# Performance work log

Measured on AMD Instinct MI355X. Metric: run time of the kernel, lower is better.

## Reference

```python
import jax, jax.numpy as jnp
import numpy as np

NO = 16          # config['Max_Object']
NT = 8           # config['Max_Time']
FEAT = 512       # config['feat_dims']
VIS_IN = 2048
TGT = 24


def setup_inputs() -> dict:
    key = jax.random.key(0)
    ks = jax.random.split(key, 10)
    b = 16
    N = NT * 2 * NO  # 256
    s = lambda k, *sh: jax.random.normal(k, sh, dtype=jnp.float32) * 0.02
    return {
        "src": jax.random.normal(ks[0], (b, 1, 1, N, VIS_IN), dtype=jnp.float32),
        "tgt_rel": jax.random.randint(ks[1], (b * NT * NO * NO,), 0, TGT, dtype=jnp.int64),
        "w1": s(ks[2], VIS_IN, FEAT), "b1": jnp.zeros((FEAT,), jnp.float32),
        "w2": s(ks[3], FEAT, FEAT),   "b2": jnp.zeros((FEAT,), jnp.float32),
        "wf": s(ks[4], FEAT, FEAT),   "bf": jnp.zeros((FEAT,), jnp.float32),
        "wr": s(ks[5], 2 * FEAT, TGT), "br": jnp.zeros((TGT,), jnp.float32),
    }


def reference(src, tgt_rel, w1, b1, w2, b2, wf, bf, wr, br):
    b = src.shape[0]
    BT = b * NT
    # src[:, 0, 0, :, :] -> (b, N, D) -> (b*NT, 2*NO, D); take visual part [:2048]
    x = src[:, 0, 0, :, :].reshape(BT, 2 * NO, -1)[:, :, :VIS_IN]
    # fc_vis: MLP 2048 -> FEAT -> FEAT
    h = jnp.maximum(x @ w1 + b1, 0.0) @ w2 + b2          # (BT, 2NO, FEAT)
    node_feats = h @ wf + bf                             # fc_fusion
    # vectorized replacement of the NOxNO python double loop:
    # edge[:, i*NO + (j-NO), :] = cat(node[:, i], node[:, j])  for i<NO<=j
    subj = jnp.broadcast_to(node_feats[:, :NO, None, :], (BT, NO, NO, FEAT))
    obj = jnp.broadcast_to(node_feats[:, None, NO:, :], (BT, NO, NO, FEAT))
    edge_feats = jnp.concatenate([subj, obj], axis=-1).reshape(BT, NO * NO, 2 * FEAT)
    out = (edge_feats @ wr + br).reshape(-1, TGT)        # fc_rel
    tgt = tgt_rel.reshape(-1)
    w_cls = jnp.asarray([1.0] + [100.0] * (TGT - 1), dtype=out.dtype)
    logp = jax.nn.log_softmax(out, axis=-1)
    nll = -jnp.take_along_axis(logp, tgt[:, None], axis=1)[:, 0]
    ww = w_cls[tgt]
    loss = jnp.sum(ww * nll) / jnp.sum(ww)  # torch weighted cross_entropy (mean)
    return out, tgt, loss
```

## Files before the change

### kernel.cpp

```cpp
#include <hip/hip_runtime.h>
#include <cstddef>
#include <cstdint>

#define NOBJ   16
#define FEAT   512
#define VIS    2048
#define NTGT   24
#define MROWS  4096
#define EROWS  32768

typedef __attribute__((ext_vector_type(8))) short short8;
typedef __attribute__((ext_vector_type(4))) float f32x4;

__device__ __forceinline__ unsigned short f2bf(float f) {
    union { float f; unsigned int i; } v; v.f = f;
    const unsigned int x = v.i;
    return (unsigned short)((x + 0x7fffu + ((x >> 16) & 1u)) >> 16);
}

__device__ __forceinline__ void gload16(const unsigned short* g, unsigned short* l) {
    __builtin_amdgcn_global_load_lds(
        (const __attribute__((address_space(1))) unsigned int*)(const void*)g,
        (__attribute__((address_space(3))) unsigned int*)(void*)l, 16, 0, 0);
}

__global__ __launch_bounds__(256)
void prep1(const float* __restrict__ w1, unsigned short* __restrict__ w1t,
           const float* __restrict__ wf, const float* __restrict__ bfv,
           const float* __restrict__ wr, float* __restrict__ t1,
           const float* __restrict__ src, unsigned short* __restrict__ srcb) {
    __shared__ float shbuf[FEAT * NTGT];
    const int b   = blockIdx.x;
    const int tid = threadIdx.x;
    if (b < 1024) {
        float (*tile)[33] = (float(*)[33])shbuf;
        const int k0 = (b & 63) * 32;
        const int n0 = (b >> 6) * 32;
        const int tx = tid & 31, ty = tid >> 5;
        #pragma unroll
        for (int r = 0; r < 32; r += 8)
            tile[ty + r][tx] = w1[(size_t)(k0 + ty + r) * FEAT + n0 + tx];
        __syncthreads();
        #pragma unroll
        for (int r = 0; r < 32; r += 8)
            w1t[(size_t)(n0 + ty + r) * VIS + k0 + tx] = f2bf(tile[tx][ty + r]);
    } else if (b < 1154) {
        const int bb = b - 1024;
        const int h  = bb & 1;
        const float* wrh = wr + (size_t)h * FEAT * NTGT;
        for (int idx = tid; idx < FEAT * NTGT; idx += 256)
            shbuf[idx] = wrh[idx];
        __syncthreads();
        const int c    = tid & 31;
        const int krow = (bb >> 1) * 8 + (tid >> 5);
        if (krow > 512) return;
        const float* rowp = (krow < 512) ? (wf + (size_t)krow * FEAT) : bfv;
        const int ce = (c < NTGT) ? c : NTGT - 1;
        float s = 0.f;
        #pragma unroll 8
        for (int j = 0; j < FEAT; ++j)
            s = fmaf(rowp[j], shbuf[j * NTGT + ce], s);
        if (c < NTGT) t1[((size_t)h * 513 + krow) * 32 + c] = s;
    } else {
        const int bb = b - 1154;
        #pragma unroll
        for (int q = 0; q < 4; ++q) {
            const size_t i = (size_t)bb * 8192 + q * 2048 + tid * 8;
            const float4 a = *reinterpret_cast<const float4*>(src + i);
            const float4 c = *reinterpret_cast<const float4*>(src + i + 4);
            short8 o;
            o[0] = (short)f2bf(a.x); o[1] = (short)f2bf(a.y);
            o[2] = (short)f2bf(a.z); o[3] = (short)f2bf(a.w);
            o[4] = (short)f2bf(c.x); o[5] = (short)f2bf(c.y);
            o[6] = (short)f2bf(c.z); o[7] = (short)f2bf(c.w);
            *reinterpret_cast<short8*>(srcb + i) = o;
        }
    }
}

__global__ __launch_bounds__(256)
void prep2(const float* __restrict__ w2, const float* __restrict__ b2,
           const float* __restrict__ t1, unsigned short* __restrict__ wABt,
           float* __restrict__ biasAB, float* __restrict__ P) {
    __shared__ float shbuf[FEAT * NTGT];
    const int b   = blockIdx.x;
    const int tid = threadIdx.x;
    if (b < 1024) {
        P[(size_t)b * 256 + tid] = 0.f;
        return;
    }
    const int bb = b - 1024;
    const int h  = bb & 1;
    for (int idx = tid; idx < FEAT * NTGT; idx += 256) {
        const int row = idx / NTGT, col = idx - row * NTGT;
        shbuf[idx] = t1[((size_t)h * 513 + row) * 32 + col];
    }
    __syncthreads();
    const int c = tid & 31;
    const int r = (bb >> 1) * 8 + (tid >> 5);
    if (r > 512) return;
    const float* rowp = (r < 512) ? (w2 + (size_t)r * FEAT) : b2;
    const int ce = (c < NTGT) ? c : NTGT - 1;
    float s = 0.f;
    #pragma unroll 8
    for (int k = 0; k < FEAT; ++k)
        s = fmaf(rowp[k], shbuf[k * NTGT + ce], s);
    if (c < NTGT) {
        const int q = h * NTGT + c;
        if (r < 512) wABt[(size_t)q * FEAT + r] = f2bf(s);
        else         biasAB[q] = s + t1[((size_t)h * 513 + 512) * 32 + c];
    }
}

__global__ __launch_bounds__(256)
void gemm1f(const unsigned short* __restrict__ srcb, const unsigned short* __restrict__ w1t,
            const float* __restrict__ b1, const unsigned short* __restrict__ wABt,
            float* __restrict__ P) {
    __shared__ __align__(16) unsigned short As[2][64 * 64];
    __shared__ __align__(16) unsigned short Bs[2][32 * 64];

    const int bid = blockIdx.x;
    const int xcd = bid & 7;
    const int k8  = bid >> 3;
    const int xb  = k8 & 15;
    const int yb  = (xcd << 3) | (k8 >> 4);
    const int m0 = yb * 64;
    const int n0 = xb * 32;

    const int tid  = threadIdx.x;
    const int lane = tid & 63;
    const int wid  = tid >> 6;
    const int wr = wid >> 1, wc = wid & 1;

    const int aRow0 = tid >> 3, aCd0 = (tid & 7) ^ (aRow0 & 7);
    const int s1i   = 256 + tid;
    const int aRow1 = s1i >> 3, aCd1 = (s1i & 7) ^ (aRow1 & 7);
    const int bN    = tid >> 3, bCd = (tid & 7) ^ (bN & 7);
    const size_t aOff0 = (size_t)(m0 + aRow0) * VIS + (aCd0 << 3);
    const size_t aOff1 = (size_t)(m0 + aRow1) * VIS + (aCd1 << 3);
    const size_t bOff  = (size_t)(n0 + bN) * VIS + (bCd << 3);
    const int ldsA0 = (wid * 64) << 3;
    const int ldsA1 = (256 + wid * 64) << 3;
    const int ldsB  = (wid * 64) << 3;

    f32x4 acc[2] = {};

    gload16(srcb + aOff0, &As[0][ldsA0]);
    gload16(srcb + aOff1, &As[0][ldsA1]);
    gload16(w1t + bOff,  &Bs[0][ldsB]);
    __syncthreads();

    int cur = 0;
    for (int t = 0; t < VIS / 64; ++t) {
        if (t + 1 < VIS / 64) {
            const int kn = (t + 1) * 64;
            gload16(srcb + aOff0 + kn, &As[cur ^ 1][ldsA0]);
            gload16(srcb + aOff1 + kn, &As[cur ^ 1][ldsA1]);
            gload16(w1t + bOff + kn,  &Bs[cur ^ 1][ldsB]);
        }
        #pragma unroll
        for (int k2 = 0; k2 < 2; ++k2) {
            short8 af[2], bfr;
            #pragma unroll
            for (int fr = 0; fr < 2; ++fr) {
                const int row = wr * 32 + fr * 16 + (lane & 15);
                const int cw  = ((k2 << 2) + (lane >> 4)) ^ (row & 7);
                af[fr] = *reinterpret_cast<const short8*>(&As[cur][(row << 6) + (cw << 3)]);
            }
            {
                const int n  = wc * 16 + (lane & 15);
                const int cw = ((k2 << 2) + (lane >> 4)) ^ (n & 7);
                bfr = *reinterpret_cast<const short8*>(&Bs[cur][(n << 6) + (cw << 3)]);
            }
            #pragma unroll
            for (int fr = 0; fr < 2; ++fr)
                acc[fr] = __builtin_amdgcn_mfma_f32_16x16x32_bf16(af[fr], bfr, acc[fr], 0, 0, 0);
        }
        __syncthreads();
        cur ^= 1;
    }

    short8 bq[3];
    #pragma unroll
    for (int t3 = 0; t3 < 3; ++t3)
        bq[t3] = *reinterpret_cast<const short8*>(
            wABt + (size_t)(t3 * 16 + (lane & 15)) * FEAT + n0 + ((lane >> 4) << 3));

    unsigned short* Ht = &As[0][0];
    {
        const int nl   = wc * 16 + (lane & 15);
        const float bias = b1[n0 + nl];
        #pragma unroll
        for (int fr = 0; fr < 2; ++fr) {
            const int ml = wr * 32 + fr * 16 + ((lane >> 4) << 2);
            #pragma unroll
            for (int r = 0; r < 4; ++r) {
                const float v = fmaxf(acc[fr][r] + bias, 0.f);
                Ht[(ml + r) * 40 + nl] = f2bf(v);
            }
        }
    }
    __syncthreads();

    short8 aep;
    {
        const int m = wid * 16 + (lane & 15);
        aep = *reinterpret_cast<const short8*>(&Ht[m * 40 + ((lane >> 4) << 3)]);
    }
    const f32x4 pz = {0.f, 0.f, 0.f, 0.f};
    #pragma unroll
    for (int t3 = 0; t3 < 3; ++t3) {
        f32x4 pp = __builtin_amdgcn_mfma_f32_16x16x32_bf16(aep, bq[t3], pz, 0, 0, 0);
        const int q  = t3 * 16 + (lane & 15);
        const int mb = m0 + wid * 16 + ((lane >> 4) << 2);
        #pragma unroll
        for (int r = 0; r < 4; ++r)
            atomicAdd(&P[(size_t)(mb + r) * 64 + q], pp[r]);
    }
}

__global__ __launch_bounds__(256)
void out_loss_kernel(const float* __restrict__ P, const float* __restrict__ br,
                     const float* __restrict__ biasAB, const int* __restrict__ tgt,
                     float* __restrict__ out, float* __restrict__ out_tgt,
                     float* __restrict__ partials) {
    __shared__ float sm[32][49];
    const int bt  = blockIdx.x;
    const int tid = threadIdx.x;
    for (int idx = tid; idx < 32 * 48; idx += 256) {
        const int row = idx / 48, col = idx - row * 48;
        sm[row][col] = P[(size_t)(bt * 32 + row) * 64 + col];
    }
    __syncthreads();

    const int r  = bt * 256 + tid;
    const int i  = tid >> 4, j = tid & 15;
    const int tg = tgt[r];

    float vals[NTGT];
    float mx = -1e30f, vtg = 0.f;
    #pragma unroll
    for (int t = 0; t < NTGT; ++t) {
        const float cv = br[t] + biasAB[t] + biasAB[24 + t];
        const float v  = sm[i][t] + sm[16 + j][24 + t] + cv;
        vals[t] = v;
        mx = fmaxf(mx, v);
        if (t == tg) vtg = v;
    }
    float se = 0.f;
    #pragma unroll
    for (int t = 0; t < NTGT; ++t) se += expf(vals[t] - mx);
    const float lse = mx + logf(se);

    float4* o4 = reinterpret_cast<float4*>(out + (size_t)r * NTGT);
    #pragma unroll
    for (int q = 0; q < 6; ++q)
        o4[q] = make_float4(vals[q * 4], vals[q * 4 + 1], vals[q * 4 + 2], vals[q * 4 + 3]);
    out_tgt[r] = (float)tg;

    const float wcl = (tg == 0) ? 1.f : 100.f;
    float p1 = wcl * (lse - vtg);
    float p2 = wcl;
    #pragma unroll
    for (int off = 32; off > 0; off >>= 1) {
        p1 += __shfl_down(p1, off);
        p2 += __shfl_down(p2, off);
    }
    __shared__ float s1[4], s2[4];
    const int lane = tid & 63, wv = tid >> 6;
    if (lane == 0) { s1[wv] = p1; s2[wv] = p2; }
    __syncthreads();
    if (tid == 0) {
        partials[bt]       = s1[0] + s1[1] + s1[2] + s1[3];
        partials[128 + bt] = s2[0] + s2[1] + s2[2] + s2[3];
    }
}

__global__ void final_loss(const float* __restrict__ partials, float* __restrict__ loss) {
    const int t = threadIdx.x;
    float a = partials[t] + partials[t + 64];
    float b = partials[128 + t] + partials[192 + t];
    #pragma unroll
    for (int off = 32; off > 0; off >>= 1) {
        a += __shfl_down(a, off);
        b += __shfl_down(b, off);
    }
    if (t == 0) loss[0] = a / b;
}

extern "C" void kernel_launch(void* const* d_in, const int* in_sizes, int n_in,
                              void* d_out, int out_size, void* d_ws, size_t ws_size,
                              hipStream_t stream) {
    const float* src = (const float*)d_in[0];
    const int*   tgt = (const int*)d_in[1];
    const float* w1  = (const float*)d_in[2];
    const float* b1  = (const float*)d_in[3];
    const float* w2  = (const float*)d_in[4];
    const float* b2  = (const float*)d_in[5];
    const float* wf  = (const float*)d_in[6];
    const float* bfv = (const float*)d_in[7];
    const float* wr  = (const float*)d_in[8];
    const float* br  = (const float*)d_in[9];

    float* ws = (float*)d_ws;
    unsigned short* w1t   = (unsigned short*)(ws);
    unsigned short* srcb  = (unsigned short*)(ws + 524288);
    float*          t1    = ws + 4718592;
    unsigned short* wABt  = (unsigned short*)(ws + 4751424);
    float*          biasAB = ws + 4763712;
    float*          P     = ws + 4763776;
    float*          parts = ws + 5025920;

    float* out_logits = (float*)d_out;
    float* out_tgt    = out_logits + (size_t)EROWS * NTGT;
    float* out_lossp  = out_tgt + EROWS;

    prep1<<<2178, 256, 0, stream>>>(w1, w1t, wf, bfv, wr, t1, src, srcb);
    prep2<<<1154, 256, 0, stream>>>(w2, b2, t1, wABt, biasAB, P);
    gemm1f<<<1024, 256, 0, stream>>>(srcb, w1t, b1, wABt, P);
    out_loss_kernel<<<128, 256, 0, stream>>>(P, br, biasAB, tgt,
                                             out_logits, out_tgt, parts);
    final_loss<<<1, 64, 0, stream>>>(parts, out_lossp);
}
```

Before: 160.8 us.

## Use 128x32 GEMM tiles with 32x32 MFMA and move P zeroing to prep1

The main GEMM tile grows from 64x32 to 128x32, so each of the four waves now owns a 32x32 output computed with the 32x32x16 bf16 MFMA instead of two 16x16x32 MFMAs. This halves the block count and the number of times each W1 column tile is reloaded, which improves operand reuse. Zeroing of the P accumulator moves from prep2 into extra prep1 blocks, leaving prep2 with only its reduction blocks. The cost is that 512 blocks may underfill the CUs and that shared memory per block is larger.

```diff
diff --git a/kernel.cpp b/kernel.cpp
--- a/kernel.cpp
+++ b/kernel.cpp
@@ -11,6 +11,7 @@
 
 typedef __attribute__((ext_vector_type(8))) short short8;
 typedef __attribute__((ext_vector_type(4))) float f32x4;
+typedef __attribute__((ext_vector_type(16))) float f32x16;
 
 __device__ __forceinline__ unsigned short f2bf(float f) {
     union { float f; unsigned int i; } v; v.f = f;
@@ -28,7 +29,8 @@
 void prep1(const float* __restrict__ w1, unsigned short* __restrict__ w1t,
            const float* __restrict__ wf, const float* __restrict__ bfv,
            const float* __restrict__ wr, float* __restrict__ t1,
-           const float* __restrict__ src, unsigned short* __restrict__ srcb) {
+           const float* __restrict__ src, unsigned short* __restrict__ srcb,
+           float* __restrict__ P) {
     __shared__ float shbuf[FEAT * NTGT];
     const int b   = blockIdx.x;
     const int tid = threadIdx.x;
@@ -61,7 +63,7 @@
         for (int j = 0; j < FEAT; ++j)
             s = fmaf(rowp[j], shbuf[j * NTGT + ce], s);
         if (c < NTGT) t1[((size_t)h * 513 + krow) * 32 + c] = s;
-    } else {
+    } else if (b < 2178) {
         const int bb = b - 1154;
         #pragma unroll
         for (int q = 0; q < 4; ++q) {
@@ -75,29 +77,27 @@
             o[6] = (short)f2bf(c.z); o[7] = (short)f2bf(c.w);
             *reinterpret_cast<short8*>(srcb + i) = o;
         }
+    } else {
+        const int bb = b - 2178;
+        P[(size_t)bb * 256 + tid] = 0.f;
     }
 }
 
 __global__ __launch_bounds__(256)
 void prep2(const float* __restrict__ w2, const float* __restrict__ b2,
            const float* __restrict__ t1, unsigned short* __restrict__ wABt,
-           float* __restrict__ biasAB, float* __restrict__ P) {
+           float* __restrict__ biasAB) {
     __shared__ float shbuf[FEAT * NTGT];
     const int b   = blockIdx.x;
     const int tid = threadIdx.x;
-    if (b < 1024) {
-        P[(size_t)b * 256 + tid] = 0.f;
-        return;
-    }
-    const int bb = b - 1024;
-    const int h  = bb & 1;
+    const int h   = b & 1;
     for (int idx = tid; idx < FEAT * NTGT; idx += 256) {
         const int row = idx / NTGT, col = idx - row * NTGT;
         shbuf[idx] = t1[((size_t)h * 513 + row) * 32 + col];
     }
     __syncthreads();
     const int c = tid & 31;
-    const int r = (bb >> 1) * 8 + (tid >> 5);
+    const int r = (b >> 1) * 8 + (tid >> 5);
     if (r > 512) return;
     const float* rowp = (r < 512) ? (w2 + (size_t)r * FEAT) : b2;
     const int ce = (c < NTGT) ? c : NTGT - 1;
@@ -116,69 +116,76 @@
 void gemm1f(const unsigned short* __restrict__ srcb, const unsigned short* __restrict__ w1t,
             const float* __restrict__ b1, const unsigned short* __restrict__ wABt,
             float* __restrict__ P) {
-    __shared__ __align__(16) unsigned short As[2][64 * 64];
+    __shared__ __align__(16) unsigned short As[2][128 * 64];
     __shared__ __align__(16) unsigned short Bs[2][32 * 64];
 
     const int bid = blockIdx.x;
     const int xcd = bid & 7;
     const int k8  = bid >> 3;
     const int xb  = k8 & 15;
-    const int yb  = (xcd << 3) | (k8 >> 4);
-    const int m0 = yb * 64;
+    const int yb  = (xcd << 2) | (k8 >> 4);
+    const int m0 = yb * 128;
     const int n0 = xb * 32;
 
     const int tid  = threadIdx.x;
     const int lane = tid & 63;
     const int wid  = tid >> 6;
-    const int wr = wid >> 1, wc = wid & 1;
-
-    const int aRow0 = tid >> 3, aCd0 = (tid & 7) ^ (aRow0 & 7);
-    const int s1i   = 256 + tid;
-    const int aRow1 = s1i >> 3, aCd1 = (s1i & 7) ^ (aRow1 & 7);
-    const int bN    = tid >> 3, bCd = (tid & 7) ^ (bN & 7);
-    const size_t aOff0 = (size_t)(m0 + aRow0) * VIS + (aCd0 << 3);
-    const size_t aOff1 = (size_t)(m0 + aRow1) * VIS + (aCd1 << 3);
-    const size_t bOff  = (size_t)(n0 + bN) * VIS + (bCd << 3);
-    const int ldsA0 = (wid * 64) << 3;
-    const int ldsA1 = (256 + wid * 64) << 3;
-    const int ldsB  = (wid * 64) << 3;
-
-    f32x4 acc[2] = {};
-
-    gload16(srcb + aOff0, &As[0][ldsA0]);
-    gload16(srcb + aOff1, &As[0][ldsA1]);
-    gload16(w1t + bOff,  &Bs[0][ldsB]);
+
+    const int aRow = tid >> 3, aCd = (tid & 7) ^ (aRow & 7);
+    const int bN   = tid >> 3, bCd = (tid & 7) ^ (bN & 7);
+    const size_t aOff = (size_t)(m0 + aRow) * VIS + (aCd << 3);
+    const size_t bOff = (size_t)(n0 + bN) * VIS + (bCd << 3);
+    const int ldsWb = (wid * 64) << 3;
+
+    f32x16 acc = {};
+
+    #pragma unroll
+    for (int q = 0; q < 4; ++q)
+        gload16(srcb + aOff + (size_t)q * 32 * VIS, &As[0][(q * 256) * 8 + ldsWb]);
+    gload16(w1t + bOff, &Bs[0][ldsWb]);
     __syncthreads();
 
     int cur = 0;
     for (int t = 0; t < VIS / 64; ++t) {
         if (t + 1 < VIS / 64) {
             const int kn = (t + 1) * 64;
-            gload16(srcb + aOff0 + kn, &As[cur ^ 1][ldsA0]);
-            gload16(srcb + aOff1 + kn, &As[cur ^ 1][ldsA1]);
-            gload16(w1t + bOff + kn,  &Bs[cur ^ 1][ldsB]);
-        }
-        #pragma unroll
-        for (int k2 = 0; k2 < 2; ++k2) {
-            short8 af[2], bfr;
             #pragma unroll
-            for (int fr = 0; fr < 2; ++fr) {
-                const int row = wr * 32 + fr * 16 + (lane & 15);
-                const int cw  = ((k2 << 2) + (lane >> 4)) ^ (row & 7);
-                af[fr] = *reinterpret_cast<const short8*>(&As[cur][(row << 6) + (cw << 3)]);
+            for (int q = 0; q < 4; ++q)
+                gload16(srcb + aOff + (size_t)q * 32 * VIS + kn,
+                        &As[cur ^ 1][(q * 256) * 8 + ldsWb]);
+            gload16(w1t + bOff + kn, &Bs[cur ^ 1][ldsWb]);
+        }
+        #pragma unroll
+        for (int k2 = 0; k2 < 4; ++k2) {
+            const int chunk = (k2 << 1) + (lane >> 5);
+            short8 af, bf8;
+            {
+                const int row = wid * 32 + (lane & 31);
+                const int cw  = chunk ^ (row & 7);
+                af = *reinterpret_cast<const short8*>(&As[cur][(row << 6) + (cw << 3)]);
             }
             {
-                const int n  = wc * 16 + (lane & 15);
-                const int cw = ((k2 << 2) + (lane >> 4)) ^ (n & 7);
-                bfr = *reinterpret_cast<const short8*>(&Bs[cur][(n << 6) + (cw << 3)]);
+                const int n  = lane & 31;
+                const int cw = chunk ^ (n & 7);
+                bf8 = *reinterpret_cast<const short8*>(&Bs[cur][(n << 6) + (cw << 3)]);
             }
-            #pragma unroll
-            for (int fr = 0; fr < 2; ++fr)
-                acc[fr] = __builtin_amdgcn_mfma_f32_16x16x32_bf16(af[fr], bfr, acc[fr], 0, 0, 0);
+            acc = __builtin_amdgcn_mfma_f32_32x32x16_bf16(af, bf8, acc, 0, 0, 0);
         }
         __syncthreads();
         cur ^= 1;
     }
+
+    unsigned short* Ht = &As[0][0];
+    {
+        const float bias = b1[n0 + (lane & 31)];
+        #pragma unroll
+        for (int r = 0; r < 16; ++r) {
+            const int row = wid * 32 + (r & 3) + ((r >> 2) << 3) + ((lane >> 5) << 2);
+            const float v = fmaxf(acc[r] + bias, 0.f);
+            Ht[row * 40 + (lane & 31)] = f2bf(v);
+        }
+    }
+    __syncthreads();
 
     short8 bq[3];
     #pragma unroll
@@ -186,36 +193,23 @@
         bq[t3] = *reinterpret_cast<const short8*>(
             wABt + (size_t)(t3 * 16 + (lane & 15)) * FEAT + n0 + ((lane >> 4) << 3));
 
-    unsigned short* Ht = &As[0][0];
-    {
-        const int nl   = wc * 16 + (lane & 15);
-        const float bias = b1[n0 + nl];
-        #pragma unroll
-        for (int fr = 0; fr < 2; ++fr) {
-            const int ml = wr * 32 + fr * 16 + ((lane >> 4) << 2);
+    const f32x4 pz = {0.f, 0.f, 0.f, 0.f};
+    #pragma unroll
+    for (int fr = 0; fr < 2; ++fr) {
+        short8 aep;
+        {
+            const int m = wid * 32 + fr * 16 + (lane & 15);
+            aep = *reinterpret_cast<const short8*>(&Ht[m * 40 + ((lane >> 4) << 3)]);
+        }
+        #pragma unroll
+        for (int t3 = 0; t3 < 3; ++t3) {
+            f32x4 pp = __builtin_amdgcn_mfma_f32_16x16x32_bf16(aep, bq[t3], pz, 0, 0, 0);
+            const int q  = t3 * 16 + (lane & 15);
+            const int mb = m0 + wid * 32 + fr * 16 + ((lane >> 4) << 2);
             #pragma unroll
-            for (int r = 0; r < 4; ++r) {
-                const float v = fmaxf(acc[fr][r] + bias, 0.f);
-                Ht[(ml + r) * 40 + nl] = f2bf(v);
-            }
-        }
-    }
-    __syncthreads();
-
-    short8 aep;
-    {
-        const int m = wid * 16 + (lane & 15);
-        aep = *reinterpret_cast<const short8*>(&Ht[m * 40 + ((lane >> 4) << 3)]);
-    }
-    const f32x4 pz = {0.f, 0.f, 0.f, 0.f};
-    #pragma unroll
-    for (int t3 = 0; t3 < 3; ++t3) {
-        f32x4 pp = __builtin_amdgcn_mfma_f32_16x16x32_bf16(aep, bq[t3], pz, 0, 0, 0);
-        const int q  = t3 * 16 + (lane & 15);
-        const int mb = m0 + wid * 16 + ((lane >> 4) << 2);
-        #pragma unroll
-        for (int r = 0; r < 4; ++r)
-            atomicAdd(&P[(size_t)(mb + r) * 64 + q], pp[r]);
+            for (int r = 0; r < 4; ++r)
+                atomicAdd(&P[(size_t)(mb + r) * 64 + q], pp[r]);
+        }
     }
 }
 
@@ -315,9 +309,9 @@
     float* out_tgt    = out_logits + (size_t)EROWS * NTGT;
     float* out_lossp  = out_tgt + EROWS;
 
-    prep1<<<2178, 256, 0, stream>>>(w1, w1t, wf, bfv, wr, t1, src, srcb);
-    prep2<<<1154, 256, 0, stream>>>(w2, b2, t1, wABt, biasAB, P);
-    gemm1f<<<1024, 256, 0, stream>>>(srcb, w1t, b1, wABt, P);
+    prep1<<<3202, 256, 0, stream>>>(w1, w1t, wf, bfv, wr, t1, src, srcb, P);
+    prep2<<<130, 256, 0, stream>>>(w2, b2, t1, wABt, biasAB);
+    gemm1f<<<512, 256, 0, stream>>>(srcb, w1t, b1, wABt, P);
     out_loss_kernel<<<128, 256, 0, stream>>>(P, br, biasAB, tgt,
                                              out_logits, out_tgt, parts);
     final_loss<<<1, 64, 0, stream>>>(parts, out_lossp);
```

Result: no change. 163.6 us (+1.8%).
